# Kernel tuning notes

Hardware: AMD Instinct MI355X
Metric: run time of the kernel (lower is better)

## Reference

```python
import jax, jax.numpy as jnp
import numpy as np

B, S, HID = 2, 2048, 2048
H, HKV, D = 16, 4, 128
BS = 64            # block_size
TAU = 0.5          # threshold_tau
NB = S // BS       # number of blocks
SCALE = 1.0 / (D ** 0.5)


def _rotate_half(x):
    x1, x2 = x[..., : D // 2], x[..., D // 2 :]
    return jnp.concatenate([-x2, x1], axis=-1)


def setup_inputs() -> dict:
    key = jax.random.key(0)
    k0, k1, k2, k3, k4 = jax.random.split(key, 5)
    hidden_states = jax.random.normal(k0, (B, S, HID), jnp.float32)
    # standard rotary embeddings, [B, S, D] (ndim==3 path of _apply_rotary_pos_emb)
    pos = jnp.arange(S, dtype=jnp.float32)
    inv_freq = 1.0 / (10000.0 ** (jnp.arange(0, D, 2, dtype=jnp.float32) / D))
    emb = jnp.concatenate([pos[:, None] * inv_freq[None, :]] * 2, axis=-1)  # [S, D]
    cos = jnp.broadcast_to(jnp.cos(emb)[None], (B, S, D)).astype(jnp.float32)
    sin = jnp.broadcast_to(jnp.sin(emb)[None], (B, S, D)).astype(jnp.float32)
    Wq = jax.random.normal(k1, (HID, H * D), jnp.float32) * 0.02
    Wk = jax.random.normal(k2, (HID, HKV * D), jnp.float32) * 0.02
    Wv = jax.random.normal(k3, (HID, HKV * D), jnp.float32) * 0.02
    Wo = jax.random.normal(k4, (HID, HID), jnp.float32) * 0.02
    return {"hidden_states": hidden_states, "cos": cos, "sin": sin,
            "Wq": Wq, "Wk": Wk, "Wv": Wv, "Wo": Wo}


def reference(hidden_states, cos, sin, Wq, Wk, Wv, Wo):
    # QKV projections -> [B, heads, S, D]
    q = (hidden_states @ Wq).reshape(B, S, H, D).transpose(0, 2, 1, 3)
    k = (hidden_states @ Wk).reshape(B, S, HKV, D).transpose(0, 2, 1, 3)
    v = (hidden_states @ Wv).reshape(B, S, HKV, D).transpose(0, 2, 1, 3)
    # RoPE (cos/sin [B,S,D] -> broadcast over heads)
    c, s = cos[:, None], sin[:, None]
    q = q * c + _rotate_half(q) * s
    k = k * c + _rotate_half(k) * s
    # GQA repeat_interleave on head dim
    n_rep = H // HKV
    k = jnp.repeat(k, n_rep, axis=1)
    v = jnp.repeat(v, n_rep, axis=1)
    # ---- AttnGate: block-mean pooled Q/K scores -> hard block mask ----
    q_blk = q.reshape(B, H, NB, BS, D).mean(axis=3)  # [B,H,NB,D]
    k_blk = k.reshape(B, H, NB, BS, D).mean(axis=3)
    gate_logits = jnp.einsum('bhid,bhjd->bhij', q_blk, k_blk) * SCALE
    hard = jax.nn.sigmoid(gate_logits) >= TAU                      # [B,H,NB,NB]
    hard = hard | jnp.eye(NB, dtype=bool)                          # keep diagonal blocks
    hard = hard & jnp.tril(jnp.ones((NB, NB), dtype=bool))         # block-causal
    # expand block mask to token level and intersect with causal mask
    tok_mask = jnp.repeat(jnp.repeat(hard, BS, axis=2), BS, axis=3)  # [B,H,S,S]
    tok_mask = tok_mask & jnp.tril(jnp.ones((S, S), dtype=bool))
    # ---- block-sparse (masked) attention ----
    scores = jnp.einsum('bhsd,bhtd->bhst', q, k) * SCALE
    scores = jnp.where(tok_mask, scores, jnp.float32(-1e30))
    probs = jax.nn.softmax(scores.astype(jnp.float32), axis=-1).astype(v.dtype)
    out = jnp.einsum('bhst,bhtd->bhsd', probs, v)
    out = out.transpose(0, 2, 1, 3).reshape(B, S, HID)
    return out @ Wo
```

## Files before the change

kernel.cpp:

```cpp
#include <hip/hip_runtime.h>
#include <stdint.h>

typedef unsigned short u16;
typedef _Float16 half8 __attribute__((ext_vector_type(8)));
typedef float floatx4 __attribute__((ext_vector_type(4)));
typedef u16 u16x4 __attribute__((ext_vector_type(4)));

#define B_ 2
#define S_ 2048
#define HID_ 2048
#define H_ 16
#define HKV_ 4
#define D_ 128
#define NB_ 32
#define SCALE_ 0.08838834764831845f
#define SC_L2 0.12753102331884178f
#define SMAX_L2 5.770780163555852f

__device__ __forceinline__ u16 f2h_bits(float f) {
  _Float16 h = (_Float16)f;
  return __builtin_bit_cast(u16, h);
}

__device__ __forceinline__ void transpose_body(const float* __restrict__ src, u16* __restrict__ dst,
                                               int Kdim, int N, int ldd, int nsplit,
                                               int k0, int n0, float (*tile)[65]) {
#pragma unroll
  for (int p = 0; p < 16; ++p) {
    int e = threadIdx.x + p * 256;
    int r = e >> 6, c = e & 63;
    tile[r][c] = src[(size_t)(k0 + r) * N + n0 + c];
  }
  __syncthreads();
#pragma unroll
  for (int p = 0; p < 16; ++p) {
    int e = threadIdx.x + p * 256;
    int k = e & 63, n = e >> 6;
    float v = tile[k][n];
    for (int s = 0; s < nsplit; ++s) {
      _Float16 hh = (_Float16)v;
      dst[(size_t)(n0 + n) * ldd + s * Kdim + k0 + k] = __builtin_bit_cast(u16, hh);
      v -= (float)hh;
    }
  }
}

__global__ __launch_bounds__(256) void k_prep(const float* __restrict__ hs, u16* __restrict__ A2,
                                              const float* __restrict__ Wq, const float* __restrict__ Wk,
                                              const float* __restrict__ Wv,
                                              u16* __restrict__ B2T, u16* __restrict__ WvT) {
  __shared__ float tile[64][65];
  int id = blockIdx.x;
  if (id < 8192) {
    int idx = id * 256 + threadIdx.x;
    int f0 = idx * 4;
    float4 v = *reinterpret_cast<const float4*>(hs + f0);
    float vv[4] = {v.x, v.y, v.z, v.w};
    u16x4 h0, h1;
#pragma unroll
    for (int e = 0; e < 4; ++e) {
      _Float16 a = (_Float16)vv[e];
      float r = vv[e] - (float)a;
      _Float16 b = (_Float16)r;
      h0[e] = __builtin_bit_cast(u16, a);
      h1[e] = __builtin_bit_cast(u16, b);
    }
    int row = f0 >> 11;
    int col = f0 & 2047;
    *reinterpret_cast<u16x4*>(A2 + (size_t)row * 4096 + col) = h0;
    *reinterpret_cast<u16x4*>(A2 + (size_t)row * 4096 + 2048 + col) = h1;
  } else if (id < 9216) {
    int t = id - 8192;
    transpose_body(Wq, B2T, 2048, 2048, 4096, 2, (t & 31) * 64, (t >> 5) * 64, tile);
  } else if (id < 9472) {
    int t = id - 9216;
    transpose_body(Wk, B2T + (size_t)2048 * 4096, 2048, 512, 4096, 2, (t & 31) * 64, (t >> 5) * 64, tile);
  } else {
    int t = id - 9472;
    transpose_body(Wv, WvT, 2048, 512, 2048, 1, (t & 31) * 64, (t >> 5) * 64, tile);
  }
}

__global__ __launch_bounds__(256) void k_transpose_split(const float* __restrict__ src, u16* __restrict__ dst,
                                                         int Kdim, int N, int ldd, int nsplit) {
  __shared__ float tile[64][65];
  transpose_body(src, dst, Kdim, N, ldd, nsplit, blockIdx.x * 64, blockIdx.y * 64, tile);
}

__global__ __launch_bounds__(256) void k_add(float4* __restrict__ out, const float4* __restrict__ p1) {
  size_t i = (size_t)blockIdx.x * 256 + threadIdx.x;
  float4 a = out[i], b = p1[i];
  out[i] = (float4){a.x + b.x, a.y + b.y, a.z + b.z, a.w + b.w};
}


#define FENCE() __builtin_amdgcn_sched_barrier(0)
#define BAR() do { FENCE(); __builtin_amdgcn_s_barrier(); FENCE(); } while (0)
#define WAITVM(N) do { FENCE(); asm volatile("s_waitcnt vmcnt(" #N ")" ::: "memory"); FENCE(); } while (0)

__device__ __forceinline__ int kmap(int map, int t) {
  return ((map >> ((t >> 5) * 4)) & 15) * 2048 + (t & 31) * 64;
}

__device__ __forceinline__ void stage_half(const u16* __restrict__ src, int sr0, int lda, int kb,
                                           u16* dst, int w, int lane) {
#pragma unroll
  for (int rr = 0; rr < 2; ++rr) {
    int chunk = rr * 8 + w;
    int row = chunk * 8 + (lane >> 3);
    int slot = (lane & 7) ^ (lane >> 3);
    const u16* gp = src + (size_t)(sr0 + row) * lda + kb + slot * 8;
    __builtin_amdgcn_global_load_lds((const __attribute__((address_space(1))) unsigned int*)gp,
                                     (__attribute__((address_space(3))) unsigned int*)(dst + chunk * 512),
                                     16, 0, 0);
  }
}

#define RD_A(mh) do { \
  _Pragma("unroll") \
  for (int m_ = 0; m_ < 4; ++m_) { \
    aF[m_][0] = *reinterpret_cast<const half8*>(&sm[(mh)*8192 + (wm*64 + m_*16 + l15)*64 + ((quad ^ l7) * 8)]); \
    aF[m_][1] = *reinterpret_cast<const half8*>(&sm[(mh)*8192 + (wm*64 + m_*16 + l15)*64 + (((4 + quad) ^ l7) * 8)]); \
  } } while (0)

#define RD_B(nh, BF) do { \
  _Pragma("unroll") \
  for (int n_ = 0; n_ < 2; ++n_) { \
    BF[n_][0] = *reinterpret_cast<const half8*>(&sm[16384 + (nh)*8192 + (wn*32 + n_*16 + l15)*64 + ((quad ^ l7) * 8)]); \
    BF[n_][1] = *reinterpret_cast<const half8*>(&sm[16384 + (nh)*8192 + (wn*32 + n_*16 + l15)*64 + (((4 + quad) ^ l7) * 8)]); \
  } } while (0)

#define MM(mh, nh, BF) do { \
  __builtin_amdgcn_s_setprio(1); \
  _Pragma("unroll") \
  for (int m_ = 0; m_ < 4; ++m_) \
  _Pragma("unroll") \
  for (int n_ = 0; n_ < 2; ++n_) { \
    acc[(mh)*4 + m_][(nh)*2 + n_] = __builtin_amdgcn_mfma_f32_16x16x32_f16(aF[m_][0], BF[n_][0], acc[(mh)*4 + m_][(nh)*2 + n_], 0, 0, 0); \
    acc[(mh)*4 + m_][(nh)*2 + n_] = __builtin_amdgcn_mfma_f32_16x16x32_f16(aF[m_][1], BF[n_][1], acc[(mh)*4 + m_][(nh)*2 + n_], 0, 0, 0); \
  } \
  __builtin_amdgcn_s_setprio(0); } while (0)

__device__ __forceinline__ void gemm256(const u16* __restrict__ A, const u16* __restrict__ BT,
                                        float* __restrict__ C, u16* __restrict__ Ch, u16* sm,
                                        int row0, int col0, int NT,
                                        int lda, int ldb, int ldc, int ldch,
                                        int amap, int bmap, int koffA, int koffB) {
  const int tid = (int)threadIdx.x;
  const int lane = tid & 63;
  const int w = tid >> 6;
  const int wm = w >> 2, wn = w & 3;
  const int quad = lane >> 4, l15 = lane & 15, l7 = lane & 7;

  floatx4 acc[8][4];
#pragma unroll
  for (int i = 0; i < 8; ++i)
#pragma unroll
    for (int j = 0; j < 4; ++j) acc[i][j] = (floatx4){0.f, 0.f, 0.f, 0.f};

  half8 aF[4][2], bF0[2][2], bF1[2][2];

  {
    int ka = kmap(amap, 0) + koffA, kb = kmap(bmap, 0) + koffB;
    stage_half(A,  row0,       lda, ka, sm + 0,     w, lane);
    stage_half(BT, col0,       ldb, kb, sm + 16384, w, lane);
    stage_half(BT, col0 + 128, ldb, kb, sm + 24576, w, lane);
    stage_half(A,  row0 + 128, lda, ka, sm + 8192,  w, lane);
  }
  WAITVM(4);
  BAR();

  for (int t = 0; t < NT; ++t) {
    int tn = t + 1; if (tn >= NT) tn = 0;
    int kan = kmap(amap, tn) + koffA, kbn = kmap(bmap, tn) + koffB;

    RD_A(0); RD_B(0, bF0);
    WAITVM(2);
    BAR(); MM(0, 0, bF0); BAR();
    RD_B(1, bF1);
    stage_half(A,  row0, lda, kan, sm + 0,     w, lane);
    stage_half(BT, col0, ldb, kbn, sm + 16384, w, lane);
    WAITVM(4);
    BAR(); MM(0, 1, bF1); BAR();
    RD_A(1);
    stage_half(BT, col0 + 128, ldb, kbn, sm + 24576, w, lane);
    BAR(); MM(1, 1, bF1); BAR();
    stage_half(A, row0 + 128, lda, kan, sm + 8192, w, lane);
    WAITVM(4);
    BAR(); MM(1, 0, bF0); BAR();
  }
  WAITVM(0);

#pragma unroll
  for (int i = 0; i < 8; ++i) {
    int mh = i >> 2, m = i & 3;
#pragma unroll
    for (int j = 0; j < 4; ++j) {
      int nh = j >> 1, n = j & 1;
#pragma unroll
      for (int r = 0; r < 4; ++r) {
        int rr = row0 + mh * 128 + wm * 64 + m * 16 + quad * 4 + r;
        int cc = col0 + nh * 128 + wn * 32 + n * 16 + l15;
        if (Ch)
          Ch[(size_t)rr * ldch + cc] = f2h_bits(acc[i][j][r]);
        else
          C[(size_t)rr * ldc + cc] = acc[i][j][r];
      }
    }
  }
}

__global__ __launch_bounds__(512) void k_gemm_qkv(const u16* __restrict__ A2, const u16* __restrict__ B2T,
                                                  const u16* __restrict__ WvT, float* __restrict__ qkv,
                                                  u16* __restrict__ corr) {
  __shared__ u16 sm[32768];
  int id = blockIdx.x;
  if (id < 160) {
    int row0 = (id / 10) * 256, col0 = (id % 10) * 256;
    gemm256(A2, B2T, nullptr, corr, sm, row0, col0, 64, 4096, 4096, 0, 2560, 0x01, 0x10, 0, 0);
  } else if (id < 320) {
    int t = id - 160;
    int row0 = (t / 10) * 256, col0 = (t % 10) * 256;
    gemm256(A2, B2T, qkv, nullptr, sm, row0, col0, 32, 4096, 4096, 3072, 0, 0, 0, 0, 0);
  } else {
    int t = id - 320;
    int row0 = (t >> 1) * 256, col0 = (t & 1) * 256;
    gemm256(A2, WvT, qkv + 2560, nullptr, sm, row0, col0, 32, 4096, 2048, 3072, 0, 0, 0, 0, 0);
  }
}

__global__ __launch_bounds__(512) void k_gemm_wo(const u16* __restrict__ attn, const u16* __restrict__ WoT,
                                                 float* __restrict__ out, float* __restrict__ P1) {
  __shared__ u16 sm[32768];
  int id = blockIdx.x;
  int p = id >> 7, rem = id & 127;
  int row0 = (rem >> 3) * 256, col0 = (rem & 7) * 256;
  float* Cp = p ? P1 : out;
  gemm256(attn, WoT, Cp, nullptr, sm, row0, col0, 16, 2048, 2048, 2048, 0, 0, 0,
          p * 1024, p * 1024);
}

__global__ __launch_bounds__(256) void k_rope_mean(const float* __restrict__ qkv, const u16* __restrict__ corr,
                                                   const float* __restrict__ cosb, const float* __restrict__ sinb,
                                                   u16* __restrict__ qbf, u16* __restrict__ kbf,
                                                   float* __restrict__ qblk, float* __restrict__ kblk) {
  int cc = blockIdx.x, i = blockIdx.y, b = blockIdx.z;
  int c = cc * 256 + threadIdx.x;
  bool isq = c < 2048;
  int hh = isq ? (c >> 7) : ((c - 2048) >> 7);
  int d = isq ? (c & 127) : ((c - 2048) & 127);
  int pairc = (d < 64) ? c + 64 : c - 64;
  float sgn = (d < 64) ? -1.0f : 1.0f;
  int row0 = b * S_ + i * 64;
  float sum = 0.0f;
  for (int s = 0; s < 64; ++s) {
    int row = row0 + s;
    float x1 = qkv[(size_t)row * 3072 + c]
             + (float)__builtin_bit_cast(_Float16, corr[(size_t)row * 2560 + c]);
    float x2 = qkv[(size_t)row * 3072 + pairc]
             + (float)__builtin_bit_cast(_Float16, corr[(size_t)row * 2560 + pairc]);
    float cv = cosb[(size_t)row * 128 + d];
    float sv = sinb[(size_t)row * 128 + d];
    float val = x1 * cv + sgn * x2 * sv;
    sum += val;
    if (isq)
      qbf[((size_t)(b * H_ + hh) * S_ + i * 64 + s) * 128 + d] = f2h_bits(val);
    else
      kbf[((size_t)(b * HKV_ + hh) * S_ + i * 64 + s) * 128 + d] = f2h_bits(val);
  }
  if (isq)
    qblk[((size_t)(b * H_ + hh) * NB_ + i) * 128 + d] = sum * 0.015625f;
  else
    kblk[((size_t)(b * HKV_ + hh) * NB_ + i) * 128 + d] = sum * 0.015625f;
}

__global__ __launch_bounds__(256) void k_vlayout(const float* __restrict__ qkv, u16* __restrict__ vT) {
  int i = blockIdx.x, hk = blockIdx.y, b = blockIdx.z;
  __shared__ u16 tile[64 * 130];
#pragma unroll
  for (int p = 0; p < 32; ++p) {
    int e = threadIdx.x + p * 256;
    int s = e >> 7, d = e & 127;
    float v = qkv[(size_t)(b * S_ + i * 64 + s) * 3072 + 2560 + hk * 128 + d];
    tile[s * 130 + d] = f2h_bits(v);
  }
  __syncthreads();
#pragma unroll
  for (int p = 0; p < 32; ++p) {
    int e = threadIdx.x + p * 256;
    int d2 = e >> 6, s2 = e & 63;
    vT[((size_t)(b * HKV_ + hk) * 128 + d2) * S_ + i * 64 + s2] = tile[s2 * 130 + d2];
  }
}

__global__ __launch_bounds__(256) void k_gate(const float* __restrict__ qblk, const float* __restrict__ kblk,
                                              int* __restrict__ mask) {
  int h = blockIdx.x, b = blockIdx.y;
  int hk = h >> 2;
  __shared__ float qs[32 * 128];
  __shared__ float ks[32 * 128];
  size_t qb0 = (size_t)(b * H_ + h) * NB_ * 128;
  size_t kb0 = (size_t)(b * HKV_ + hk) * NB_ * 128;
#pragma unroll
  for (int p = 0; p < 16; ++p) {
    int e = threadIdx.x + p * 256;
    qs[e] = qblk[qb0 + e];
    ks[e] = kblk[kb0 + e];
  }
  __syncthreads();
#pragma unroll
  for (int p = 0; p < 4; ++p) {
    int l = threadIdx.x + p * 256;
    int i = l >> 5, j = l & 31;
    int m;
    if (j > i) m = 0;
    else if (j == i) m = 1;
    else {
      float dot = 0.0f;
      for (int d = 0; d < 128; ++d) dot += qs[i * 128 + d] * ks[j * 128 + d];
      m = (dot >= 0.0f) ? 1 : 0;
    }
    mask[((size_t)(b * H_ + h) * NB_ + i) * NB_ + j] = m;
  }
}

__global__ __launch_bounds__(256) void k_flash(const u16* __restrict__ qbf, const u16* __restrict__ kbf,
                                               const u16* __restrict__ vT, const int* __restrict__ mask,
                                               u16* __restrict__ attn) {
  const int id = blockIdx.x;
  const int i = 31 - (id >> 5);
  const int hb = id & 31;
  const int h = hb & 15, b = hb >> 4;
  const int hk = h >> 2;
  const int tid = threadIdx.x;
  const int lane = tid & 63;
  const int w = tid >> 6;
  const int quad = lane >> 4;
  const int l15 = lane & 15;

  __shared__ u16 Ksb[2 * 64 * 128];
  __shared__ u16 Vsb[2 * 128 * 64];
  __shared__ u16 Ps[4 * 16 * 64];

  half8 qF[4];
  const u16* qbase = qbf + ((size_t)(b * H_ + h) * S_ + i * 64 + w * 16 + l15) * 128;
#pragma unroll
  for (int kk = 0; kk < 4; ++kk)
    qF[kk] = *reinterpret_cast<const half8*>(qbase + kk * 32 + quad * 8);

  floatx4 o[8];
#pragma unroll
  for (int t = 0; t < 8; ++t) o[t] = (floatx4){0.f, 0.f, 0.f, 0.f};
  float ls[4] = {0.f, 0.f, 0.f, 0.f};

  const u16* kb = kbf + (size_t)(b * HKV_ + hk) * S_ * 128;
  const u16* vb = vT + (size_t)(b * HKV_ + hk) * 128 * S_;
  const int* mrp = mask + ((size_t)(b * H_ + h) * NB_ + i) * NB_;

#define FSTAGE(J, BUF) do { \
  _Pragma("unroll") \
  for (int t_ = 0; t_ < 4; ++t_) { \
    int g2 = t_ * 4 + w; \
    int stok = g2 * 4 + (lane >> 4); \
    int ul = (lane & 15) ^ (stok & 15); \
    const u16* srcK = kb + (size_t)((J) * 64 + stok) * 128 + ul * 8; \
    __builtin_amdgcn_global_load_lds((const __attribute__((address_space(1))) unsigned int*)srcK, \
                                     (__attribute__((address_space(3))) unsigned int*)(Ksb + (BUF) * 8192 + g2 * 512), \
                                     16, 0, 0); \
    int sdd = g2 * 8 + (lane >> 3); \
    int ulv = (lane & 7) ^ (sdd & 7); \
    const u16* srcV = vb + (size_t)sdd * S_ + (J) * 64 + ulv * 8; \
    __builtin_amdgcn_global_load_lds((const __attribute__((address_space(1))) unsigned int*)srcV, \
                                     (__attribute__((address_space(3))) unsigned int*)(Vsb + (BUF) * 8192 + g2 * 512), \
                                     16, 0, 0); \
  } } while (0)

  int jcur = 0;
  while (!mrp[jcur]) ++jcur;
  FSTAGE(jcur, 0);
  int cur = 0;

  for (;;) {
    int jn = jcur + 1;
    while (jn <= i && !mrp[jn]) ++jn;
    bool hn = (jn <= i);
    if (hn) { FSTAGE(jn, cur ^ 1); WAITVM(8); }
    else    { WAITVM(0); }
    BAR();

    const u16* Kc = Ksb + cur * 8192;
    const u16* Vc = Vsb + cur * 8192;
#pragma unroll
    for (int ct = 0; ct < 4; ++ct) {
      floatx4 cacc = (floatx4){0.f, 0.f, 0.f, 0.f};
#pragma unroll
      for (int kk = 0; kk < 4; ++kk) {
        int phys = (kk * 4 + quad) ^ l15;
        half8 bF = *reinterpret_cast<const half8*>(&Kc[(ct * 16 + l15) * 128 + phys * 8]);
        cacc = __builtin_amdgcn_mfma_f32_16x16x32_f16(qF[kk], bF, cacc, 0, 0, 0);
      }
#pragma unroll
      for (int r = 0; r < 4; ++r) {
        float s = cacc[r];
        if (jcur == i && (ct * 16 + l15) > (w * 16 + quad * 4 + r)) s = -1e30f;
        float p = __builtin_exp2f(fmaf(s, SC_L2, -SMAX_L2));
        _Float16 ph = (_Float16)p;
        ls[r] += (float)ph;
        Ps[w * 1024 + (quad * 4 + r) * 64 + ct * 16 + l15] = __builtin_bit_cast(u16, ph);
      }
    }
#pragma unroll
    for (int kk2 = 0; kk2 < 2; ++kk2) {
      half8 aP = *reinterpret_cast<const half8*>(&Ps[w * 1024 + l15 * 64 + kk2 * 32 + quad * 8]);
#pragma unroll
      for (int ct2 = 0; ct2 < 8; ++ct2) {
        int phys = (kk2 * 4 + quad) ^ (l15 & 7);
        half8 bV = *reinterpret_cast<const half8*>(&Vc[(ct2 * 16 + l15) * 64 + phys * 8]);
        o[ct2] = __builtin_amdgcn_mfma_f32_16x16x32_f16(aP, bV, o[ct2], 0, 0, 0);
      }
    }
    BAR();
    if (!hn) break;
    jcur = jn; cur ^= 1;
  }

#pragma unroll
  for (int xm = 1; xm < 16; xm <<= 1)
#pragma unroll
    for (int r = 0; r < 4; ++r) ls[r] += __shfl_xor(ls[r], xm, 64);
  float invl[4];
#pragma unroll
  for (int r = 0; r < 4; ++r) invl[r] = 1.0f / ls[r];
#pragma unroll
  for (int ct2 = 0; ct2 < 8; ++ct2)
#pragma unroll
    for (int r = 0; r < 4; ++r) {
      size_t row = (size_t)(b * S_ + i * 64 + w * 16 + quad * 4 + r);
      attn[row * 2048 + h * 128 + ct2 * 16 + l15] = f2h_bits(o[ct2][r] * invl[r]);
    }
}

extern "C" void kernel_launch(void* const* d_in, const int* in_sizes, int n_in,
                              void* d_out, int out_size, void* d_ws, size_t ws_size,
                              hipStream_t stream) {
  const float* hs = (const float*)d_in[0];
  const float* cosb = (const float*)d_in[1];
  const float* sinb = (const float*)d_in[2];
  const float* Wq = (const float*)d_in[3];
  const float* Wk = (const float*)d_in[4];
  const float* Wv = (const float*)d_in[5];
  const float* Wo = (const float*)d_in[6];
  float* out = (float*)d_out;
  char* ws = (char*)d_ws;

  u16* A2 = (u16*)(ws + 0);
  u16* B2T = (u16*)(ws + 33554432);
  u16* WvT = (u16*)(ws + 54525952);
  float* qkv = (float*)(ws + 56623104);
  u16* corr = (u16*)out;
  u16* attn = (u16*)(ws + 0);
  u16* qbf = (u16*)(ws + 16777216);
  u16* kbf = (u16*)(ws + 33554432);
  u16* vTbf = (u16*)(ws + 37748736);
  float* qblk = (float*)(ws + 41943040);
  float* kblk = (float*)(ws + 42467328);
  int* mask = (int*)(ws + 42598400);
  u16* WoT = (u16*)(ws + 43122688);
  float* P1 = (float*)(ws + 56623104);

  (void)in_sizes; (void)n_in; (void)out_size; (void)ws_size;

  k_prep<<<9728, 256, 0, stream>>>(hs, A2, Wq, Wk, Wv, B2T, WvT);

  k_gemm_qkv<<<352, 512, 0, stream>>>(A2, B2T, WvT, qkv, corr);

  k_transpose_split<<<dim3(32, 32), 256, 0, stream>>>(Wo, WoT, 2048, 2048, 2048, 1);

  k_rope_mean<<<dim3(10, 32, 2), 256, 0, stream>>>(qkv, corr, cosb, sinb, qbf, kbf, qblk, kblk);
  k_vlayout<<<dim3(32, 4, 2), 256, 0, stream>>>(qkv, vTbf);

  k_gate<<<dim3(16, 2), 256, 0, stream>>>(qblk, kblk, mask);

  k_flash<<<1024, 256, 0, stream>>>(qbf, kbf, vTbf, mask, attn);

  k_gemm_wo<<<256, 512, 0, stream>>>(attn, WoT, out, P1);
  k_add<<<8192, 256, 0, stream>>>((float4*)out, (const float4*)P1);
}
```

Before: 405.0 us.

## Replace split-K Wo GEMM with 128x256 tiles, drop add kernel, swizzle QKV blocks

The output projection used a split-K of 2 over 256x256 tiles, writing a partial into a workspace buffer and then summing it with a separate add kernel. It now runs a new 128x256-tile GEMM over the full K range, so the same 256 blocks write the output directly, with no partial buffer and no extra launch. The QKV GEMM block index is also remapped, with an (id&7)*20 + (id>>3) permutation, to change which tiles run concurrently, likely for cache locality across XCDs. Smaller tiles lower arithmetic intensity per block, and each block now runs a longer K loop.

Result: faster. 388.5 us (-4.1%).

```diff
diff --git a/kernel.cpp b/kernel.cpp
--- a/kernel.cpp
+++ b/kernel.cpp
@@ -87,12 +87,6 @@
   transpose_body(src, dst, Kdim, N, ldd, nsplit, blockIdx.x * 64, blockIdx.y * 64, tile);
 }
 
-__global__ __launch_bounds__(256) void k_add(float4* __restrict__ out, const float4* __restrict__ p1) {
-  size_t i = (size_t)blockIdx.x * 256 + threadIdx.x;
-  float4 a = out[i], b = p1[i];
-  out[i] = (float4){a.x + b.x, a.y + b.y, a.z + b.z, a.w + b.w};
-}
-
 
 #define FENCE() __builtin_amdgcn_sched_barrier(0)
 #define BAR() do { FENCE(); __builtin_amdgcn_s_barrier(); FENCE(); } while (0)
@@ -145,7 +139,7 @@
                                         float* __restrict__ C, u16* __restrict__ Ch, u16* sm,
                                         int row0, int col0, int NT,
                                         int lda, int ldb, int ldc, int ldch,
-                                        int amap, int bmap, int koffA, int koffB) {
+                                        int amap, int bmap) {
   const int tid = (int)threadIdx.x;
   const int lane = tid & 63;
   const int w = tid >> 6;
@@ -161,7 +155,7 @@
   half8 aF[4][2], bF0[2][2], bF1[2][2];
 
   {
-    int ka = kmap(amap, 0) + koffA, kb = kmap(bmap, 0) + koffB;
+    int ka = kmap(amap, 0), kb = kmap(bmap, 0);
     stage_half(A,  row0,       lda, ka, sm + 0,     w, lane);
     stage_half(BT, col0,       ldb, kb, sm + 16384, w, lane);
     stage_half(BT, col0 + 128, ldb, kb, sm + 24576, w, lane);
@@ -172,7 +166,7 @@
 
   for (int t = 0; t < NT; ++t) {
     int tn = t + 1; if (tn >= NT) tn = 0;
-    int kan = kmap(amap, tn) + koffA, kbn = kmap(bmap, tn) + koffB;
+    int kan = kmap(amap, tn), kbn = kmap(bmap, tn);
 
     RD_A(0); RD_B(0, bF0);
     WAITVM(2);
@@ -210,34 +204,130 @@
   }
 }
 
+
+__device__ __forceinline__ void stage_halfA64(const u16* __restrict__ src, int sr0, int lda, int kb,
+                                              u16* dst, int w, int lane) {
+  int row = w * 8 + (lane >> 3);
+  int slot = (lane & 7) ^ (lane >> 3);
+  const u16* gp = src + (size_t)(sr0 + row) * lda + kb + slot * 8;
+  __builtin_amdgcn_global_load_lds((const __attribute__((address_space(1))) unsigned int*)gp,
+                                   (__attribute__((address_space(3))) unsigned int*)(dst + w * 512),
+                                   16, 0, 0);
+}
+
+#define RD_A128(mh) do { \
+  _Pragma("unroll") \
+  for (int m_ = 0; m_ < 2; ++m_) { \
+    aF[m_][0] = *reinterpret_cast<const half8*>(&sm[(mh)*4096 + (wm*32 + m_*16 + l15)*64 + ((quad ^ l7) * 8)]); \
+    aF[m_][1] = *reinterpret_cast<const half8*>(&sm[(mh)*4096 + (wm*32 + m_*16 + l15)*64 + (((4 + quad) ^ l7) * 8)]); \
+  } } while (0)
+
+#define RD_B128(nh, BF) do { \
+  _Pragma("unroll") \
+  for (int n_ = 0; n_ < 2; ++n_) { \
+    BF[n_][0] = *reinterpret_cast<const half8*>(&sm[8192 + (nh)*8192 + (wn*32 + n_*16 + l15)*64 + ((quad ^ l7) * 8)]); \
+    BF[n_][1] = *reinterpret_cast<const half8*>(&sm[8192 + (nh)*8192 + (wn*32 + n_*16 + l15)*64 + (((4 + quad) ^ l7) * 8)]); \
+  } } while (0)
+
+#define MM128(mh, nh, BF) do { \
+  __builtin_amdgcn_s_setprio(1); \
+  _Pragma("unroll") \
+  for (int m_ = 0; m_ < 2; ++m_) \
+  _Pragma("unroll") \
+  for (int n_ = 0; n_ < 2; ++n_) { \
+    acc[(mh)*2 + m_][(nh)*2 + n_] = __builtin_amdgcn_mfma_f32_16x16x32_f16(aF[m_][0], BF[n_][0], acc[(mh)*2 + m_][(nh)*2 + n_], 0, 0, 0); \
+    acc[(mh)*2 + m_][(nh)*2 + n_] = __builtin_amdgcn_mfma_f32_16x16x32_f16(aF[m_][1], BF[n_][1], acc[(mh)*2 + m_][(nh)*2 + n_], 0, 0, 0); \
+  } \
+  __builtin_amdgcn_s_setprio(0); } while (0)
+
+__device__ __forceinline__ void gemm128(const u16* __restrict__ A, const u16* __restrict__ BT,
+                                        float* __restrict__ C, u16* sm,
+                                        int row0, int col0, int NT,
+                                        int lda, int ldb, int ldc) {
+  const int tid = (int)threadIdx.x;
+  const int lane = tid & 63;
+  const int w = tid >> 6;
+  const int wm = w >> 2, wn = w & 3;
+  const int quad = lane >> 4, l15 = lane & 15, l7 = lane & 7;
+
+  floatx4 acc[4][4];
+#pragma unroll
+  for (int i = 0; i < 4; ++i)
+#pragma unroll
+    for (int j = 0; j < 4; ++j) acc[i][j] = (floatx4){0.f, 0.f, 0.f, 0.f};
+
+  half8 aF[2][2], bF0[2][2], bF1[2][2];
+
+  stage_halfA64(A,  row0,      lda, 0, sm + 0,     w, lane);
+  stage_half  (BT, col0,       ldb, 0, sm + 8192,  w, lane);
+  stage_half  (BT, col0 + 128, ldb, 0, sm + 16384, w, lane);
+  stage_halfA64(A,  row0 + 64, lda, 0, sm + 4096,  w, lane);
+  WAITVM(3);
+  BAR();
+
+  for (int t = 0; t < NT; ++t) {
+    int tn = t + 1; if (tn >= NT) tn = 0;
+    int kn = tn * 64;
+
+    RD_A128(0); RD_B128(0, bF0);
+    WAITVM(1);
+    BAR(); MM128(0, 0, bF0); BAR();
+    RD_B128(1, bF1);
+    stage_halfA64(A,  row0, lda, kn, sm + 0,    w, lane);
+    stage_half  (BT, col0, ldb, kn, sm + 8192,  w, lane);
+    WAITVM(3);
+    BAR(); MM128(0, 1, bF1); BAR();
+    RD_A128(1);
+    stage_half(BT, col0 + 128, ldb, kn, sm + 16384, w, lane);
+    BAR(); MM128(1, 1, bF1); BAR();
+    stage_halfA64(A, row0 + 64, lda, kn, sm + 4096, w, lane);
+    WAITVM(3);
+    BAR(); MM128(1, 0, bF0); BAR();
+  }
+  WAITVM(0);
+
+#pragma unroll
+  for (int i = 0; i < 4; ++i) {
+    int mh = i >> 1, m = i & 1;
+#pragma unroll
+    for (int j = 0; j < 4; ++j) {
+      int nh = j >> 1, n = j & 1;
+#pragma unroll
+      for (int r = 0; r < 4; ++r) {
+        int rr = row0 + mh * 64 + wm * 32 + m * 16 + quad * 4 + r;
+        int cc = col0 + nh * 128 + wn * 32 + n * 16 + l15;
+        C[(size_t)rr * ldc + cc] = acc[i][j][r];
+      }
+    }
+  }
+}
+
 __global__ __launch_bounds__(512) void k_gemm_qkv(const u16* __restrict__ A2, const u16* __restrict__ B2T,
                                                   const u16* __restrict__ WvT, float* __restrict__ qkv,
                                                   u16* __restrict__ corr) {
   __shared__ u16 sm[32768];
   int id = blockIdx.x;
   if (id < 160) {
-    int row0 = (id / 10) * 256, col0 = (id % 10) * 256;
-    gemm256(A2, B2T, nullptr, corr, sm, row0, col0, 64, 4096, 4096, 0, 2560, 0x01, 0x10, 0, 0);
+    int lg = (id & 7) * 20 + (id >> 3);
+    int row0 = (lg / 10) * 256, col0 = (lg % 10) * 256;
+    gemm256(A2, B2T, nullptr, corr, sm, row0, col0, 64, 4096, 4096, 0, 2560, 0x01, 0x10);
   } else if (id < 320) {
     int t = id - 160;
-    int row0 = (t / 10) * 256, col0 = (t % 10) * 256;
-    gemm256(A2, B2T, qkv, nullptr, sm, row0, col0, 32, 4096, 4096, 3072, 0, 0, 0, 0, 0);
+    int lg = (t & 7) * 20 + (t >> 3);
+    int row0 = (lg / 10) * 256, col0 = (lg % 10) * 256;
+    gemm256(A2, B2T, qkv, nullptr, sm, row0, col0, 32, 4096, 4096, 3072, 0, 0, 0);
   } else {
     int t = id - 320;
     int row0 = (t >> 1) * 256, col0 = (t & 1) * 256;
-    gemm256(A2, WvT, qkv + 2560, nullptr, sm, row0, col0, 32, 4096, 2048, 3072, 0, 0, 0, 0, 0);
+    gemm256(A2, WvT, qkv + 2560, nullptr, sm, row0, col0, 32, 4096, 2048, 3072, 0, 0, 0);
   }
 }
 
 __global__ __launch_bounds__(512) void k_gemm_wo(const u16* __restrict__ attn, const u16* __restrict__ WoT,
-                                                 float* __restrict__ out, float* __restrict__ P1) {
-  __shared__ u16 sm[32768];
+                                                 float* __restrict__ out) {
+  __shared__ u16 sm[24576];
   int id = blockIdx.x;
-  int p = id >> 7, rem = id & 127;
-  int row0 = (rem >> 3) * 256, col0 = (rem & 7) * 256;
-  float* Cp = p ? P1 : out;
-  gemm256(attn, WoT, Cp, nullptr, sm, row0, col0, 16, 2048, 2048, 2048, 0, 0, 0,
-          p * 1024, p * 1024);
+  gemm128(attn, WoT, out, sm, (id >> 3) * 128, (id & 7) * 256, 32, 2048, 2048, 2048);
 }
 
 __global__ __launch_bounds__(256) void k_rope_mean(const float* __restrict__ qkv, const u16* __restrict__ corr,
@@ -466,7 +556,6 @@
   float* kblk = (float*)(ws + 42467328);
   int* mask = (int*)(ws + 42598400);
   u16* WoT = (u16*)(ws + 43122688);
-  float* P1 = (float*)(ws + 56623104);
 
   (void)in_sizes; (void)n_in; (void)out_size; (void)ws_size;
 
@@ -483,6 +572,5 @@
 
   k_flash<<<1024, 256, 0, stream>>>(qbf, kbf, vTbf, mask, attn);
 
-  k_gemm_wo<<<256, 512, 0, stream>>>(attn, WoT, out, P1);
-  k_add<<<8192, 256, 0, stream>>>((float4*)out, (const float4*)P1);
-}
+  k_gemm_wo<<<256, 512, 0, stream>>>(attn, WoT, out);
+}
```
